# Kernel tuning notes

Hardware: AMD Instinct MI355X
Metric: run time of the kernel (lower is better)

## Reference

```python
import jax, jax.numpy as jnp
import numpy as np
import math

NUM_BUCKETS = 32
MAX_DISTANCE = 128
NUM_HEADS = 16
D_MODEL = 1024
HEAD_DIM = D_MODEL // NUM_HEADS


def _relative_position_bucket(relative_position, num_buckets=NUM_BUCKETS, max_distance=MAX_DISTANCE):
    # bidirectional=False path of the original
    rp = -jnp.minimum(relative_position, 0)  # non-negative distances
    max_exact = num_buckets // 2
    is_small = rp < max_exact
    rp_safe = jnp.maximum(rp, 1).astype(jnp.float32)
    rp_if_large = max_exact + (
        jnp.log(rp_safe / max_exact) / math.log(max_distance / max_exact) * (num_buckets - max_exact)
    ).astype(jnp.int32)
    rp_if_large = jnp.minimum(rp_if_large, num_buckets - 1)
    return jnp.where(is_small, rp, rp_if_large)


def relative_bias(rab_weight, q_len, k_len):
    ctx = jnp.arange(q_len)[:, None]
    mem = jnp.arange(k_len)[None, :]
    buckets = _relative_position_bucket(mem - ctx)  # [Q, K]
    vals = rab_weight[buckets]                       # [Q, K, H]
    return jnp.transpose(vals, (2, 0, 1))[None]      # [1, H, Q, K]


def setup_inputs() -> dict:
    key = jax.random.key(0)
    k1, k2, k3, k4 = jax.random.split(key, 4)
    B, S = 4, 2048
    return {
        "v": jax.random.normal(k1, (B, S, D_MODEL), dtype=jnp.float32),
        "k": jax.random.normal(k2, (B, S, D_MODEL), dtype=jnp.float32),
        "q": jax.random.normal(k3, (B, S, D_MODEL), dtype=jnp.float32),
        "rab_weight": jax.random.normal(k4, (NUM_BUCKETS, NUM_HEADS), dtype=jnp.float32),
    }


def reference(v, k, q, rab_weight):
    B, S, _ = q.shape
    def split(x):
        return jnp.transpose(x.reshape(B, S, NUM_HEADS, HEAD_DIM), (0, 2, 1, 3))  # [B,H,S,D]
    qh, kh, vh = split(q), split(k), split(v)
    scores = jnp.einsum("bhqd,bhkd->bhqk", qh, kh)          # [B,H,S,S]
    scores = scores + relative_bias(rab_weight, S, S)        # add relative bias
    av = jnp.einsum("bhqk,bhkd->bhqd", jax.nn.silu(scores), vh)
    return jnp.transpose(av, (0, 2, 1, 3)).reshape(B, S, D_MODEL)
```

## Files before the change

kernel.cpp:

```cpp
#include <hip/hip_runtime.h>

#define SEQ 2048
#define NH 16
#define HD 64
#define DMODEL 1024

typedef short bf16x8 __attribute__((ext_vector_type(8)));
typedef float f32x16 __attribute__((ext_vector_type(16)));

union FragU {
    bf16x8 v;
    uint4 u4;
    uint2 u2[2];
    unsigned int w[4];
    unsigned short s[8];
};

#if __has_builtin(__builtin_amdgcn_cvt_pk_bf16_f32)
typedef __bf16 v2bf_t __attribute__((ext_vector_type(2)));
__device__ __forceinline__ unsigned int pack_bf16(float lo, float hi) {
    union { v2bf_t h; unsigned int u; } cv;
    cv.h = __builtin_amdgcn_cvt_pk_bf16_f32(lo, hi);
    return cv.u;
}
#else
__device__ __forceinline__ unsigned int pack_bf16(float lo, float hi) {
    unsigned int a = __float_as_uint(lo) + 0x8000u;
    unsigned int b = __float_as_uint(hi) + 0x8000u;
    return __builtin_amdgcn_perm(b, a, 0x07060302);
}
#endif

typedef __attribute__((address_space(1))) const unsigned int glob_u32;
typedef __attribute__((address_space(3))) unsigned int lds_u32;
__device__ __forceinline__ void dma16(const unsigned short* g, unsigned short* l) {
    __builtin_amdgcn_global_load_lds((glob_u32*)g, (lds_u32*)l, 16, 0, 0);
}

#define EXP_SCALE 1.44269504f
#define LN2       0.69314718f

__global__ __launch_bounds__(256)
void prep_kernel(const float* __restrict__ Kg, const float* __restrict__ Vg,
                 unsigned short* __restrict__ wsK, unsigned short* __restrict__ wsVt)
{
    __shared__ unsigned short T[64 * 68];
    const int tid = threadIdx.x;
    const int blk = blockIdx.x;
    const int bh  = blk >> 5;
    const int it  = blk & 31;
    const int b = bh >> 4, h = bh & 15;
    const size_t inbase = (size_t)(b * SEQ + it * 64) * DMODEL + h * HD;

    #pragma unroll
    for (int i = 0; i < 2; ++i) {
        int item = tid + i * 256;
        int row = item >> 3, g = item & 7;
        const float* src = Kg + inbase + (size_t)row * DMODEL + g * 8;
        float4 x0 = *(const float4*)src;
        float4 x1 = *(const float4*)(src + 4);
        uint4 w;
        w.x = pack_bf16(x0.x, x0.y); w.y = pack_bf16(x0.z, x0.w);
        w.z = pack_bf16(x1.x, x1.y); w.w = pack_bf16(x1.z, x1.w);
        size_t dst = (size_t)(bh * 2048 + it * 64 + row) * 64 + ((g ^ (row & 7)) * 8);
        *(uint4*)&wsK[dst] = w;
    }
    {
        const int kc4 = tid >> 4, d4 = tid & 15;
        float4 a[4];
        #pragma unroll
        for (int r = 0; r < 4; ++r)
            a[r] = *(const float4*)(Vg + inbase + (size_t)(kc4 * 4 + r) * DMODEL + d4 * 4);
        const float* af = (const float*)a;
        #pragma unroll
        for (int c = 0; c < 4; ++c) {
            *(unsigned int*)&T[(d4 * 4 + c) * 68 + kc4 * 4]     = pack_bf16(af[0 * 4 + c], af[1 * 4 + c]);
            *(unsigned int*)&T[(d4 * 4 + c) * 68 + kc4 * 4 + 2] = pack_bf16(af[2 * 4 + c], af[3 * 4 + c]);
        }
    }
    __syncthreads();
    #pragma unroll
    for (int i = 0; i < 2; ++i) {
        int item = tid + i * 256;
        int d = item >> 3, g = item & 7;
        uint2 lo = *(const uint2*)&T[d * 68 + g * 8];
        uint2 hi = *(const uint2*)&T[d * 68 + g * 8 + 4];
        uint4 w; w.x = lo.x; w.y = lo.y; w.z = hi.x; w.w = hi.y;
        size_t dst = (size_t)(bh * 32 + it) * 4096 + d * 64 + ((g ^ (d & 7)) * 8);
        *(uint4*)&wsVt[dst] = w;
    }
}

__global__ __launch_bounds__(512, 4)
void paa_main(const unsigned short* __restrict__ wsK, const unsigned short* __restrict__ wsVt,
              const float* __restrict__ Qg, const float* __restrict__ RW,
              float* __restrict__ Og)
{
    __shared__ __align__(16) unsigned short KsT[2 * 4096];
    __shared__ __align__(16) unsigned short VtT[2 * 4096];
    __shared__ float btab[128];

    const int tid  = threadIdx.x;
    const int lane = tid & 63;
    const int wave = tid >> 6;
    const int half = lane >> 5;
    const int l31  = lane & 31;
    const int c7   = l31 & 7;

    const int bid  = blockIdx.x;
    const int bh   = bid & 63;
    const int qt   = bid >> 6;
    const int b    = bh >> 4;
    const int head = bh & 15;
    const int q0w  = qt * 256 + wave * 32;

    if (tid < 128) {
        int rp = tid;
        int bucket;
        if (rp < 16) bucket = rp;
        else {
            int big = 16 + (int)(logf((float)rp * 0.0625f) * 7.6943736f);
            bucket = big < 31 ? big : 31;
        }
        btab[tid] = RW[bucket * NH + head] * EXP_SCALE;
    }

    const unsigned short* kIt = wsK  + (size_t)bh * 131072 + wave * 512 + lane * 8;
    const unsigned short* vIt = wsVt + (size_t)bh * 131072 + wave * 512 + lane * 8;

    dma16(kIt, &KsT[wave * 512]);
    dma16(vIt, &VtT[wave * 512]);

    FragU qf[4];
    {
        const float* qrow = Qg + (size_t)(b * SEQ + q0w + l31) * DMODEL + head * HD;
        #pragma unroll
        for (int kf = 0; kf < 4; ++kf) {
            int dd = kf * 16 + half * 8;
            float4 x0 = *(const float4*)(qrow + dd);
            float4 x1 = *(const float4*)(qrow + dd + 4);
            FragU f;
            f.w[0] = pack_bf16(x0.x * EXP_SCALE, x0.y * EXP_SCALE);
            f.w[1] = pack_bf16(x0.z * EXP_SCALE, x0.w * EXP_SCALE);
            f.w[2] = pack_bf16(x1.x * EXP_SCALE, x1.y * EXP_SCALE);
            f.w[3] = pack_bf16(x1.z * EXP_SCALE, x1.w * EXP_SCALE);
            qf[kf] = f;
        }
    }

    f32x16 oacc[2];
    #pragma unroll
    for (int n = 0; n < 2; ++n)
        #pragma unroll
        for (int r = 0; r < 16; ++r) oacc[n][r] = 0.0f;

    __syncthreads();
    const float bias_d0  = btab[0];
    const float bias_far = btab[127];

    const int kaP = l31 * 64 + c7 * 8;
    const int vfP = l31 * 64 + c7 * 8 + half * 4;

    auto compute_tile = [&](const int BUF, const int it) {
        const int kcb = it * 64;
        const unsigned short* kb = &KsT[BUF * 4096];
        const unsigned short* vb = &VtT[BUF * 4096];
        FragU pf[4];
        #pragma unroll
        for (int t = 0; t < 2; ++t) {
            const int kcmin = kcb + t * 32;
            FragU ka[4];
            #pragma unroll
            for (int kf = 0; kf < 4; ++kf) {
                int g8 = (2 * kf + half) * 8;
                ka[kf].u4 = *(const uint4*)&kb[t * 2048 + (kaP ^ g8)];
            }
            int tcase = (q0w + 31 <= kcmin) ? 0 : ((q0w - (kcmin + 31) >= 113) ? 1 : 2);
            tcase = __builtin_amdgcn_readfirstlane(tcase);
            f32x16 st;
            if (tcase == 0) {
                #pragma unroll
                for (int r = 0; r < 16; ++r) st[r] = bias_d0;
            } else if (tcase == 1) {
                #pragma unroll
                for (int r = 0; r < 16; ++r) st[r] = bias_far;
            } else {
                const int dql = q0w + l31 - kcmin - 4 * half;
                #pragma unroll
                for (int r = 0; r < 16; ++r) {
                    int dv = dql - ((r & 3) + 8 * (r >> 2));
                    dv = dv < 0 ? 0 : (dv > 127 ? 127 : dv);
                    st[r] = btab[dv];
                }
            }
            #pragma unroll
            for (int kf = 0; kf < 4; ++kf)
                st = __builtin_amdgcn_mfma_f32_32x32x16_bf16(ka[kf].v, qf[kf].v, st, 0, 0, 0);

            float vals[16];
            #pragma unroll
            for (int r = 0; r < 16; ++r) {
                float x = st[r];
                float e = __builtin_amdgcn_exp2f(-x);
                vals[r] = x * __builtin_amdgcn_rcpf(1.0f + e);
            }
            #pragma unroll
            for (int j = 0; j < 4; ++j)
                pf[t * 2].w[j]     = pack_bf16(vals[2 * j], vals[2 * j + 1]);
            #pragma unroll
            for (int j = 0; j < 4; ++j)
                pf[t * 2 + 1].w[j] = pack_bf16(vals[8 + 2 * j], vals[9 + 2 * j]);
        }

        #pragma unroll
        for (int f = 0; f < 4; ++f) {
            #pragma unroll
            for (int n = 0; n < 2; ++n) {
                FragU vf;
                const int base = n * 2048;
                vf.u2[0] = *(const uint2*)&vb[base + (vfP ^ (2 * f * 8))];
                vf.u2[1] = *(const uint2*)&vb[base + (vfP ^ ((2 * f + 1) * 8))];
                oacc[n] = __builtin_amdgcn_mfma_f32_32x32x16_bf16(pf[f].v, vf.v, oacc[n], 0, 0, 0);
            }
        }
    };

    for (int it2 = 0; it2 < 16; ++it2) {
        const int it = it2 * 2;
        kIt += 4096; vIt += 4096;
        dma16(kIt, &KsT[4096 + wave * 512]);
        dma16(vIt, &VtT[4096 + wave * 512]);
        compute_tile(0, it);
        __syncthreads();
        if (it2 < 15) {
            kIt += 4096; vIt += 4096;
            dma16(kIt, &KsT[wave * 512]);
            dma16(vIt, &VtT[wave * 512]);
        }
        compute_tile(1, it + 1);
        __syncthreads();
    }

    float* obase = Og + (size_t)(b * SEQ) * DMODEL + head * HD;
    #pragma unroll
    for (int r = 0; r < 16; ++r) {
        int q = q0w + (r & 3) + 8 * (r >> 2) + 4 * half;
        float* orow = obase + (size_t)q * DMODEL;
        #pragma unroll
        for (int n = 0; n < 2; ++n)
            orow[n * 32 + l31] = oacc[n][r] * LN2;
    }
}

extern "C" void kernel_launch(void* const* d_in, const int* in_sizes, int n_in,
                              void* d_out, int out_size, void* d_ws, size_t ws_size,
                              hipStream_t stream) {
    const float* v  = (const float*)d_in[0];
    const float* k  = (const float*)d_in[1];
    const float* q  = (const float*)d_in[2];
    const float* rw = (const float*)d_in[3];
    float* out = (float*)d_out;
    unsigned short* wsK  = (unsigned short*)d_ws;
    unsigned short* wsVt = wsK + (size_t)4 * NH * SEQ * HD;
    prep_kernel<<<dim3(2048), dim3(256), 0, stream>>>(k, v, wsK, wsVt);
    paa_main<<<dim3(512), dim3(512), 0, stream>>>(wsK, wsVt, q, rw, out);
}
```

Measured before the change: 231.7 us.

## Pre-layout K/V into MFMA fragment order and load directly from global

The prep kernel now writes K and V^T in the exact per-lane MFMA fragment order, so the main kernel can read each operand with a single 16-byte global load per lane. This removes the LDS double buffer, the global-to-LDS DMA and the block-wide barriers. The key loop is also split into three ranges (far bias, banded bias, constant near bias), so the per-tile case test goes away. Each wave now streams K/V from global or L2 on its own with no sharing through LDS, which raises the L2 traffic per block and exposes load latency without explicit prefetching.

```diff
diff --git a/kernel.cpp b/kernel.cpp
--- a/kernel.cpp
+++ b/kernel.cpp
@@ -31,12 +31,6 @@
 }
 #endif
 
-typedef __attribute__((address_space(1))) const unsigned int glob_u32;
-typedef __attribute__((address_space(3))) unsigned int lds_u32;
-__device__ __forceinline__ void dma16(const unsigned short* g, unsigned short* l) {
-    __builtin_amdgcn_global_load_lds((glob_u32*)g, (lds_u32*)l, 16, 0, 0);
-}
-
 #define EXP_SCALE 1.44269504f
 #define LN2       0.69314718f
 
@@ -44,13 +38,15 @@
 void prep_kernel(const float* __restrict__ Kg, const float* __restrict__ Vg,
                  unsigned short* __restrict__ wsK, unsigned short* __restrict__ wsVt)
 {
-    __shared__ unsigned short T[64 * 68];
+    __shared__ unsigned short Tk[64 * 68];
+    __shared__ unsigned short Tv[64 * 68];
     const int tid = threadIdx.x;
     const int blk = blockIdx.x;
     const int bh  = blk >> 5;
     const int it  = blk & 31;
     const int b = bh >> 4, h = bh & 15;
     const size_t inbase = (size_t)(b * SEQ + it * 64) * DMODEL + h * HD;
+    const size_t obase  = (size_t)(bh * 32 + it) * 4096;
 
     #pragma unroll
     for (int i = 0; i < 2; ++i) {
@@ -59,11 +55,11 @@
         const float* src = Kg + inbase + (size_t)row * DMODEL + g * 8;
         float4 x0 = *(const float4*)src;
         float4 x1 = *(const float4*)(src + 4);
-        uint4 w;
-        w.x = pack_bf16(x0.x, x0.y); w.y = pack_bf16(x0.z, x0.w);
-        w.z = pack_bf16(x1.x, x1.y); w.w = pack_bf16(x1.z, x1.w);
-        size_t dst = (size_t)(bh * 2048 + it * 64 + row) * 64 + ((g ^ (row & 7)) * 8);
-        *(uint4*)&wsK[dst] = w;
+        uint2 w0, w1;
+        w0.x = pack_bf16(x0.x, x0.y); w0.y = pack_bf16(x0.z, x0.w);
+        w1.x = pack_bf16(x1.x, x1.y); w1.y = pack_bf16(x1.z, x1.w);
+        *(uint2*)&Tk[row * 68 + g * 8]     = w0;
+        *(uint2*)&Tk[row * 68 + g * 8 + 4] = w1;
     }
     {
         const int kc4 = tid >> 4, d4 = tid & 15;
@@ -74,20 +70,36 @@
         const float* af = (const float*)a;
         #pragma unroll
         for (int c = 0; c < 4; ++c) {
-            *(unsigned int*)&T[(d4 * 4 + c) * 68 + kc4 * 4]     = pack_bf16(af[0 * 4 + c], af[1 * 4 + c]);
-            *(unsigned int*)&T[(d4 * 4 + c) * 68 + kc4 * 4 + 2] = pack_bf16(af[2 * 4 + c], af[3 * 4 + c]);
+            *(unsigned int*)&Tv[(d4 * 4 + c) * 68 + kc4 * 4]     = pack_bf16(af[0 * 4 + c], af[1 * 4 + c]);
+            *(unsigned int*)&Tv[(d4 * 4 + c) * 68 + kc4 * 4 + 2] = pack_bf16(af[2 * 4 + c], af[3 * 4 + c]);
         }
     }
     __syncthreads();
+
     #pragma unroll
     for (int i = 0; i < 2; ++i) {
-        int item = tid + i * 256;
-        int d = item >> 3, g = item & 7;
-        uint2 lo = *(const uint2*)&T[d * 68 + g * 8];
-        uint2 hi = *(const uint2*)&T[d * 68 + g * 8 + 4];
-        uint4 w; w.x = lo.x; w.y = lo.y; w.z = hi.x; w.w = hi.y;
-        size_t dst = (size_t)(bh * 32 + it) * 4096 + d * 64 + ((g ^ (d & 7)) * 8);
-        *(uint4*)&wsVt[dst] = w;
+        int o = tid + i * 256;
+        int lane_o = o & 63, tk = o >> 6;
+        int t = tk >> 2, kf = tk & 3;
+        int half_o = lane_o >> 5, l31_o = lane_o & 31;
+        int pos = (t * 32 + l31_o) * 68 + kf * 16 + half_o * 8;
+        uint2 a0 = *(const uint2*)&Tk[pos];
+        uint2 a1 = *(const uint2*)&Tk[pos + 4];
+        uint4 w; w.x = a0.x; w.y = a0.y; w.z = a1.x; w.w = a1.y;
+        *(uint4*)&wsK[obase + (size_t)o * 8] = w;
+    }
+    #pragma unroll
+    for (int i = 0; i < 2; ++i) {
+        int o = tid + i * 256;
+        int lane_o = o & 63, fn = o >> 6;
+        int f = fn >> 1, n = fn & 1;
+        int half_o = lane_o >> 5, l31_o = lane_o & 31;
+        int d = n * 32 + l31_o;
+        int p0 = d * 68 + f * 16 + half_o * 4;
+        uint2 a0 = *(const uint2*)&Tv[p0];
+        uint2 a1 = *(const uint2*)&Tv[p0 + 8];
+        uint4 w; w.x = a0.x; w.y = a0.y; w.z = a1.x; w.w = a1.y;
+        *(uint4*)&wsVt[obase + (size_t)o * 8] = w;
     }
 }
 
@@ -96,8 +108,6 @@
               const float* __restrict__ Qg, const float* __restrict__ RW,
               float* __restrict__ Og)
 {
-    __shared__ __align__(16) unsigned short KsT[2 * 4096];
-    __shared__ __align__(16) unsigned short VtT[2 * 4096];
     __shared__ float btab[128];
 
     const int tid  = threadIdx.x;
@@ -105,7 +115,6 @@
     const int wave = tid >> 6;
     const int half = lane >> 5;
     const int l31  = lane & 31;
-    const int c7   = l31 & 7;
 
     const int bid  = blockIdx.x;
     const int bh   = bid & 63;
@@ -124,12 +133,6 @@
         }
         btab[tid] = RW[bucket * NH + head] * EXP_SCALE;
     }
-
-    const unsigned short* kIt = wsK  + (size_t)bh * 131072 + wave * 512 + lane * 8;
-    const unsigned short* vIt = wsVt + (size_t)bh * 131072 + wave * 512 + lane * 8;
-
-    dma16(kIt, &KsT[wave * 512]);
-    dma16(vIt, &VtT[wave * 512]);
 
     FragU qf[4];
     {
@@ -158,87 +161,65 @@
     const float bias_d0  = btab[0];
     const float bias_far = btab[127];
 
-    const int kaP = l31 * 64 + c7 * 8;
-    const int vfP = l31 * 64 + c7 * 8 + half * 4;
-
-    auto compute_tile = [&](const int BUF, const int it) {
-        const int kcb = it * 64;
-        const unsigned short* kb = &KsT[BUF * 4096];
-        const unsigned short* vb = &VtT[BUF * 4096];
-        FragU pf[4];
-        #pragma unroll
-        for (int t = 0; t < 2; ++t) {
-            const int kcmin = kcb + t * 32;
-            FragU ka[4];
-            #pragma unroll
-            for (int kf = 0; kf < 4; ++kf) {
-                int g8 = (2 * kf + half) * 8;
-                ka[kf].u4 = *(const uint4*)&kb[t * 2048 + (kaP ^ g8)];
-            }
-            int tcase = (q0w + 31 <= kcmin) ? 0 : ((q0w - (kcmin + 31) >= 113) ? 1 : 2);
-            tcase = __builtin_amdgcn_readfirstlane(tcase);
-            f32x16 st;
-            if (tcase == 0) {
-                #pragma unroll
-                for (int r = 0; r < 16; ++r) st[r] = bias_d0;
-            } else if (tcase == 1) {
-                #pragma unroll
-                for (int r = 0; r < 16; ++r) st[r] = bias_far;
-            } else {
-                const int dql = q0w + l31 - kcmin - 4 * half;
-                #pragma unroll
-                for (int r = 0; r < 16; ++r) {
-                    int dv = dql - ((r & 3) + 8 * (r >> 2));
-                    dv = dv < 0 ? 0 : (dv > 127 ? 127 : dv);
-                    st[r] = btab[dv];
-                }
-            }
-            #pragma unroll
-            for (int kf = 0; kf < 4; ++kf)
-                st = __builtin_amdgcn_mfma_f32_32x32x16_bf16(ka[kf].v, qf[kf].v, st, 0, 0, 0);
-
-            float vals[16];
-            #pragma unroll
-            for (int r = 0; r < 16; ++r) {
-                float x = st[r];
-                float e = __builtin_amdgcn_exp2f(-x);
-                vals[r] = x * __builtin_amdgcn_rcpf(1.0f + e);
-            }
-            #pragma unroll
-            for (int j = 0; j < 4; ++j)
-                pf[t * 2].w[j]     = pack_bf16(vals[2 * j], vals[2 * j + 1]);
-            #pragma unroll
-            for (int j = 0; j < 4; ++j)
-                pf[t * 2 + 1].w[j] = pack_bf16(vals[8 + 2 * j], vals[9 + 2 * j]);
-        }
-
-        #pragma unroll
-        for (int f = 0; f < 4; ++f) {
+    const unsigned short* kp = wsK  + (size_t)bh * 131072 + lane * 8;
+    const unsigned short* vp = wsVt + (size_t)bh * 131072 + lane * 8;
+
+    auto do_half = [&](const f32x16& cbias) {
+        FragU ka[4];
+        #pragma unroll
+        for (int kf = 0; kf < 4; ++kf)
+            ka[kf].u4 = *(const uint4*)(kp + kf * 512);
+        f32x16 st = __builtin_amdgcn_mfma_f32_32x32x16_bf16(ka[0].v, qf[0].v, cbias, 0, 0, 0);
+        #pragma unroll
+        for (int kf = 1; kf < 4; ++kf)
+            st = __builtin_amdgcn_mfma_f32_32x32x16_bf16(ka[kf].v, qf[kf].v, st, 0, 0, 0);
+        FragU pf[2];
+        #pragma unroll
+        for (int r = 0; r < 8; ++r) {
+            float x0 = st[2 * r], x1 = st[2 * r + 1];
+            float p0 = x0 * __builtin_amdgcn_rcpf(1.0f + __builtin_amdgcn_exp2f(-x0));
+            float p1 = x1 * __builtin_amdgcn_rcpf(1.0f + __builtin_amdgcn_exp2f(-x1));
+            pf[r >> 2].w[r & 3] = pack_bf16(p0, p1);
+        }
+        #pragma unroll
+        for (int fo = 0; fo < 2; ++fo)
             #pragma unroll
             for (int n = 0; n < 2; ++n) {
                 FragU vf;
-                const int base = n * 2048;
-                vf.u2[0] = *(const uint2*)&vb[base + (vfP ^ (2 * f * 8))];
-                vf.u2[1] = *(const uint2*)&vb[base + (vfP ^ ((2 * f + 1) * 8))];
-                oacc[n] = __builtin_amdgcn_mfma_f32_32x32x16_bf16(pf[f].v, vf.v, oacc[n], 0, 0, 0);
+                vf.u4 = *(const uint4*)(vp + fo * 1024 + n * 512);
+                oacc[n] = __builtin_amdgcn_mfma_f32_32x32x16_bf16(pf[fo].v, vf.v, oacc[n], 0, 0, 0);
             }
-        }
+        kp += 2048; vp += 2048;
     };
 
-    for (int it2 = 0; it2 < 16; ++it2) {
-        const int it = it2 * 2;
-        kIt += 4096; vIt += 4096;
-        dma16(kIt, &KsT[4096 + wave * 512]);
-        dma16(vIt, &VtT[4096 + wave * 512]);
-        compute_tile(0, it);
-        __syncthreads();
-        if (it2 < 15) {
-            kIt += 4096; vIt += 4096;
-            dma16(kIt, &KsT[wave * 512]);
-            dma16(vIt, &VtT[wave * 512]);
-        }
-        compute_tile(1, it + 1);
-        __syncthreads();
+    int htFar = (q0w - 112) >> 5; if (htFar < 0) htFar = 0;
+    int htD0  = (q0w + 62) >> 5;  if (htD0 > 64) htD0 = 64;
+
+    {
+        f32x16 cb;
+        #pragma unroll
+        for (int r = 0; r < 16; ++r) cb[r] = bias_far;
+        for (int ht = 0; ht < htFar; ++ht) do_half(cb);
+    }
+    {
+        for (int ht = htFar; ht < htD0; ++ht) {
+            const int kcmin = ht * 32;
+            f32x16 bs;
+            const int dql = q0w + l31 - kcmin - 4 * half;
+            #pragma unroll
+            for (int r = 0; r < 16; ++r) {
+                int dv = dql - ((r & 3) + 8 * (r >> 2));
+                dv = dv < 0 ? 0 : (dv > 127 ? 127 : dv);
+                bs[r] = btab[dv];
+            }
+            do_half(bs);
+        }
+    }
+    {
+        f32x16 cb;
+        #pragma unroll
+        for (int r = 0; r < 16; ++r) cb[r] = bias_d0;
+        for (int ht = htD0; ht < 64; ++ht) do_half(cb);
     }
 
     float* obase = Og + (size_t)(b * SEQ) * DMODEL + head * HD;
```

After: 224.0 us. -3.3%, faster.
